# Optimization experiments

Hardware: AMD Instinct MI355X
Metric: run time of the kernel (lower is better)

The kernel has to match this reference:

```python
import jax, jax.numpy as jnp
import numpy as np
from jax import lax

B, N, C = 1, 4096, 256
NUM_HEADS, TOP_K = 8, 8
HID = 4 * C  # MSFN hidden_dim
EPS = 1e-5


def layer_norm(x, g, b):
    mu = jnp.mean(x, axis=-1, keepdims=True)
    var = jnp.mean((x - mu) ** 2, axis=-1, keepdims=True)
    return (x - mu) / jnp.sqrt(var + EPS) * g + b


def dwconv(x, w, b, pad):
    # x: [B,C,H,W]; w: [O,1,k,k] with feature_group_count=C (torch groups=dim)
    y = lax.conv_general_dilated(x, w, (1, 1), [(pad, pad), (pad, pad)],
                                 feature_group_count=C,
                                 dimension_numbers=("NCHW", "OIHW", "NCHW"))
    return y + b[None, :, None, None]


def setup_inputs() -> dict:
    key = jax.random.key(0)
    ks = jax.random.split(key, 12)
    std = 0.02
    inp = {
        "x": jax.random.normal(ks[0], (B, N, C), jnp.float32),
        "H": 64,
        "W": 64,
        "ln1_g": jnp.ones((C,), jnp.float32),
        "ln1_b": jnp.zeros((C,), jnp.float32),
        "q_w": jax.random.normal(ks[1], (C, C), jnp.float32) * std,
        "q_b": jnp.zeros((C,), jnp.float32),
        "kv_w": jax.random.normal(ks[2], (C, 2 * C), jnp.float32) * std,
        "kv_b": jnp.zeros((2 * C,), jnp.float32),
        "proj_w": jax.random.normal(ks[3], (C, C), jnp.float32) * std,
        "proj_b": jnp.zeros((C,), jnp.float32),
        "ln2_g": jnp.ones((C,), jnp.float32),
        "ln2_b": jnp.zeros((C,), jnp.float32),
        "conv3_w": jax.random.normal(ks[4], (HID, 1, 3, 3), jnp.float32) * np.sqrt(2.0 / (HID * 9 / C)),
        "conv3_b": jnp.zeros((HID,), jnp.float32),
        "conv5_w": jax.random.normal(ks[5], (HID, 1, 5, 5), jnp.float32) * np.sqrt(2.0 / (HID * 25 / C)),
        "conv5_b": jnp.zeros((HID,), jnp.float32),
        "conv1_w": jax.random.normal(ks[6], (C, 2 * HID, 1, 1), jnp.float32) * np.sqrt(2.0 / (C + 2 * HID)),
        "conv1_b": jnp.zeros((C,), jnp.float32),
    }
    return inp


def reference(x, H, W, ln1_g, ln1_b, q_w, q_b, kv_w, kv_b, proj_w, proj_b,
              ln2_g, ln2_b, conv3_w, conv3_b, conv5_w, conv5_b, conv1_w, conv1_b):
    Bh, Nn, Cc = x.shape
    D = Cc // NUM_HEADS
    scale = D ** -0.5

    # --- Dynamic sparse attention ---
    h = layer_norm(x, ln1_g, ln1_b)
    q = jax.nn.relu((h @ q_w + q_b).reshape(Bh, Nn, NUM_HEADS, D).transpose(0, 2, 1, 3))
    kv = (h @ kv_w + kv_b).reshape(Bh, Nn, 2, NUM_HEADS, D).transpose(2, 0, 3, 1, 4)
    k, v = kv[0], kv[1]  # [B,heads,N,D]
    attn = jnp.einsum("bhnd,bhmd->bhnm", q, k) * scale  # full dense map
    _, idx = lax.top_k(attn, TOP_K)  # [B,heads,N,k]
    bi = jnp.arange(Bh)[:, None, None, None]
    hi = jnp.arange(NUM_HEADS)[None, :, None, None]
    ni = jnp.arange(Nn)[None, None, :, None]
    mask = jnp.zeros_like(attn).at[bi, hi, ni, idx].set(1.0)
    # NOTE: matches torch exactly: non-topk entries become 0 (not -inf) pre-softmax
    sa = jax.nn.softmax(attn * mask, axis=-1)
    out = jnp.einsum("bhnm,bhmd->bhnd", sa, v).transpose(0, 2, 1, 3).reshape(Bh, Nn, Cc)
    x = x + (out @ proj_w + proj_b)

    # --- MSFN ---
    h2 = layer_norm(x, ln2_g, ln2_b)
    img = h2.transpose(0, 2, 1).reshape(Bh, Cc, H, W)
    x3 = jax.nn.relu(dwconv(img, conv3_w, conv3_b, 1))
    x5 = jax.nn.relu(dwconv(img, conv5_w, conv5_b, 2))
    cat = jnp.concatenate([x3, x5], axis=1)
    y = lax.conv_general_dilated(cat, conv1_w, (1, 1), [(0, 0), (0, 0)],
                                 dimension_numbers=("NCHW", "OIHW", "NCHW"))
    y = y + conv1_b[None, :, None, None]
    x = x + y.reshape(Bh, Cc, Nn).transpose(0, 2, 1)
    return x
```

## Files before the change

### kernel.cpp

```cpp
#include <hip/hip_runtime.h>
#include <math.h>

#define N_TOK 4096
#define C_DIM 256
#define HEADS 8
#define HDIM  32
#define SCALE 0.17677669529663687f

typedef float f32x4 __attribute__((ext_vector_type(4)));
typedef float f32x2 __attribute__((ext_vector_type(2)));
typedef int   i32x4 __attribute__((ext_vector_type(4)));
typedef __bf16 bf16x8 __attribute__((ext_vector_type(8)));
typedef __bf16 bf16x2 __attribute__((ext_vector_type(2)));

#if defined(__has_builtin)
#if __has_builtin(__builtin_amdgcn_mfma_f32_16x16x32_bf16)
#define HAVE_MFMA_BUILTIN 1
#endif
#if __has_builtin(__builtin_amdgcn_fdot2_f32_bf16)
#define HAVE_DOT2 1
#endif
#endif

__device__ __forceinline__ unsigned short f2bf(float x){
  unsigned u = __float_as_uint(x);
  u += 0x7FFFu + ((u >> 16) & 1u);
  return (unsigned short)(u >> 16);
}

__device__ __forceinline__ size_t pk_idx(int m, int k, int KT){
  return ((size_t)(m >> 4)*KT + (k >> 5))*512 + (((m & 15) + 16*((k >> 3) & 3))*8 + (k & 7));
}

__device__ __forceinline__ unsigned f2key(float s){
  unsigned b = __float_as_uint(s);
  return b ^ ((unsigned)((int)b >> 31) | 0x80000000u);
}
__device__ __forceinline__ unsigned umax_(unsigned a, unsigned b){ return a > b ? a : b; }
__device__ __forceinline__ unsigned umin_(unsigned a, unsigned b){ return a < b ? a : b; }

#define KCMP(A,i,j) { unsigned h_ = umax_(A[i],A[j]); unsigned l_ = umin_(A[i],A[j]); A[i]=h_; A[j]=l_; }

__device__ __forceinline__ void sort8(unsigned (&k)[8]){
  KCMP(k,0,1) KCMP(k,2,3) KCMP(k,4,5) KCMP(k,6,7)
  KCMP(k,0,2) KCMP(k,1,3) KCMP(k,4,6) KCMP(k,5,7)
  KCMP(k,1,2) KCMP(k,5,6)
  KCMP(k,0,4) KCMP(k,1,5) KCMP(k,2,6) KCMP(k,3,7)
  KCMP(k,2,4) KCMP(k,3,5)
  KCMP(k,1,2) KCMP(k,3,4) KCMP(k,5,6)
}

__device__ __forceinline__ void mergetop8(unsigned (&a)[8], const unsigned (&b)[8]){
  #pragma unroll
  for (int j=0;j<8;++j) a[j] = umax_(a[j], b[7-j]);
  KCMP(a,0,4) KCMP(a,1,5) KCMP(a,2,6) KCMP(a,3,7)
  KCMP(a,0,2) KCMP(a,1,3) KCMP(a,4,6) KCMP(a,5,7)
  KCMP(a,0,1) KCMP(a,2,3) KCMP(a,4,5) KCMP(a,6,7)
}

template<int MLO, int MHI>
__device__ __forceinline__ void merge_keys(unsigned (&k)[8]){
  #pragma unroll
  for (int m=MLO; m<=MHI; m<<=1){
    unsigned o[8];
    #pragma unroll
    for (int j=0;j<8;++j) o[j] = (unsigned)__shfl_xor((int)k[j], m);
    #pragma unroll
    for (int j=0;j<8;++j) k[j] = umax_(k[j], o[7-j]);
    KCMP(k,0,4) KCMP(k,1,5) KCMP(k,2,6) KCMP(k,3,7)
    KCMP(k,0,2) KCMP(k,1,3) KCMP(k,4,6) KCMP(k,5,7)
    KCMP(k,0,1) KCMP(k,2,3) KCMP(k,4,5) KCMP(k,6,7)
  }
}

__device__ __forceinline__ f32x4 mfma16(i32x4 a, i32x4 b, f32x4 c){
#ifdef HAVE_MFMA_BUILTIN
  return __builtin_amdgcn_mfma_f32_16x16x32_bf16(
      __builtin_bit_cast(bf16x8, a), __builtin_bit_cast(bf16x8, b), c, 0, 0, 0);
#else
  f32x4 d;
  asm volatile("v_mfma_f32_16x16x32_bf16 %0, %1, %2, %3\n\ts_nop 7\n\ts_nop 3"
               : "=&v"(d) : "v"(a), "v"(b), "v"(c));
  return d;
#endif
}

#ifdef HAVE_DOT2
struct QCtx { unsigned q[16]; };
__device__ __forceinline__ void qload(QCtx& qc, const unsigned short* qrow){
  #pragma unroll
  for (int i=0;i<4;++i){
    i32x4 qv = *(const i32x4*)(qrow + i*8);
    #pragma unroll
    for (int j=0;j<4;++j) qc.q[i*4+j] = (unsigned)qv[j];
  }
}
__device__ __forceinline__ float dot32(const i32x4& k0, const i32x4& k1,
                                       const i32x4& k2, const i32x4& k3, const QCtx& qc){
  float s = 0.f;
  #pragma unroll
  for (int q=0;q<4;++q){
    const i32x4& kv = (q==0)?k0 : (q==1)?k1 : (q==2)?k2 : k3;
    #pragma unroll
    for (int j=0;j<4;++j)
      s = __builtin_amdgcn_fdot2_f32_bf16(__builtin_bit_cast(bf16x2, (unsigned)kv[j]),
                                          __builtin_bit_cast(bf16x2, qc.q[q*4+j]), s, false);
  }
  return s;
}
#else
struct QCtx { f32x2 q[16]; };
__device__ __forceinline__ void qload(QCtx& qc, const unsigned short* qrow){
  #pragma unroll
  for (int i=0;i<4;++i){
    i32x4 qv = *(const i32x4*)(qrow + i*8);
    #pragma unroll
    for (int j=0;j<4;++j){
      unsigned u = (unsigned)qv[j];
      f32x2 p; p.x = __uint_as_float(u << 16); p.y = __uint_as_float(u & 0xFFFF0000u);
      qc.q[i*4+j] = p;
    }
  }
}
__device__ __forceinline__ float dot32(const i32x4& k0, const i32x4& k1,
                                       const i32x4& k2, const i32x4& k3, const QCtx& qc){
  f32x2 acc = {0.f, 0.f};
  #pragma unroll
  for (int q=0;q<4;++q){
    const i32x4& kv = (q==0)?k0 : (q==1)?k1 : (q==2)?k2 : k3;
    #pragma unroll
    for (int j=0;j<4;++j){
      unsigned u = (unsigned)kv[j];
      f32x2 p; p.x = __uint_as_float(u << 16); p.y = __uint_as_float(u & 0xFFFF0000u);
      acc += p * qc.q[q*4+j];
    }
  }
  return acc.x + acc.y;
}
#endif

template<int TO_PACK>
__global__ __launch_bounds__(256) void ln_kernel(const float* __restrict__ x,
    const float* __restrict__ g, const float* __restrict__ b,
    float* __restrict__ outF, unsigned short* __restrict__ outP)
{
  int row = blockIdx.x, c = threadIdx.x;
  float v = x[(size_t)row*C_DIM + c];
  float s1 = v, s2 = v*v;
  #pragma unroll
  for (int off=1; off<64; off<<=1){
    s1 += __shfl_xor(s1, off);
    s2 += __shfl_xor(s2, off);
  }
  __shared__ float r1[4], r2[4];
  int wv = c >> 6;
  if ((c & 63) == 0){ r1[wv] = s1; r2[wv] = s2; }
  __syncthreads();
  s1 = r1[0]+r1[1]+r1[2]+r1[3];
  s2 = r2[0]+r2[1]+r2[2]+r2[3];
  float mu  = s1 * (1.0f/C_DIM);
  float var = s2 * (1.0f/C_DIM) - mu*mu;
  float inv = 1.0f / sqrtf(var + 1e-5f);
  float o = (v - mu) * inv * g[c] + b[c];
  if (TO_PACK) outP[pk_idx(row, c, 8)] = f2bf(o);
  else         outF[(size_t)row*C_DIM + c] = o;
}

__global__ __launch_bounds__(256) void transpose_k(const float* __restrict__ src,
    float* __restrict__ dstF, int R, int Cc)
{
  __shared__ float t[64][65];
  int c0 = blockIdx.x*64, r0 = blockIdx.y*64;
  int x = threadIdx.x & 63, ys = threadIdx.x >> 6;
  #pragma unroll
  for (int i=0;i<16;++i){
    int r = ys + i*4;
    t[r][x] = src[(size_t)(r0+r)*Cc + c0 + x];
  }
  __syncthreads();
  #pragma unroll
  for (int i=0;i<16;++i){
    int rr = ys + i*4;
    dstF[(size_t)(c0+rr)*R + r0 + x] = t[x][rr];
  }
}

__global__ __launch_bounds__(256) void transpose_pack(const float* __restrict__ src,
    unsigned short* __restrict__ dstP, int Cc, int nbase, int KT)
{
  __shared__ float t[64][65];
  int c0 = blockIdx.x*64, r0 = blockIdx.y*64;
  int x = threadIdx.x & 63, ys = threadIdx.x >> 6;
  #pragma unroll
  for (int i=0;i<16;++i){
    int r = ys + i*4;
    t[r][x] = src[(size_t)(r0+r)*Cc + c0 + x];
  }
  __syncthreads();
  #pragma unroll
  for (int i=0;i<16;++i){
    int rr = ys + i*4;
    int n = nbase + c0 + rr;
    int k = r0 + x;
    dstP[pk_idx(n, k, KT)] = f2bf(t[x][rr]);
  }
}

__global__ __launch_bounds__(256) void pack_w1(const float* __restrict__ w1,
                                               unsigned short* __restrict__ w1p)
{
  int blk = blockIdx.x;
  int tid = threadIdx.x;
  int lane = tid >> 2;
  int j = (tid & 3) * 2;
  int n = (blk >> 6)*16 + (lane & 15);
  int k = (blk & 63)*32 + (lane >> 4)*8 + j;
  unsigned lo = f2bf(w1[(size_t)n*2048 + k]);
  unsigned hi = f2bf(w1[(size_t)n*2048 + k + 1]);
  *(unsigned*)(w1p + (size_t)blk*512 + lane*8 + j) = lo | (hi << 16);
}

#define LDT(p, i) (*(const i32x4*)((p) + (size_t)(i)*512))

template<int KTT, int KTC, int NPAIR>
__global__ __launch_bounds__(128, 2) void gemm_packed(
    const unsigned short* __restrict__ Ap, const unsigned short* __restrict__ Bp,
    const float* __restrict__ bias, const float* __restrict__ resid,
    float* __restrict__ outF, float* __restrict__ pbuf)
{
  int wave = threadIdx.x >> 6, lane = threadIdx.x & 63;
  int l16 = lane & 15, lg = lane >> 4;
  int mt = blockIdx.x*2 + wave;
  int nt0 = blockIdx.y * NPAIR;
  int z = blockIdx.z;
  const unsigned short* ap  = Ap + ((size_t)mt*KTT  + z*KTC)*512 + lane*8;
  const unsigned short* bp0 = Bp + ((size_t)nt0*KTT + z*KTC)*512 + lane*8;
  const unsigned short* bp1 = Bp + ((size_t)(nt0+1)*KTT + z*KTC)*512 + lane*8;
  f32x4 acc0 = {0.f,0.f,0.f,0.f}, acc1 = acc0;

  i32x4 A0 = LDT(ap,0), A1 = LDT(ap,1), A2 = LDT(ap,2), A3 = LDT(ap,3);
  i32x4 B0 = LDT(bp0,0), B1 = LDT(bp0,1), B2 = LDT(bp0,2), B3 = LDT(bp0,3);
  i32x4 C0, C1, C2, C3;
  if (NPAIR == 2){ C0 = LDT(bp1,0); C1 = LDT(bp1,1); C2 = LDT(bp1,2); C3 = LDT(bp1,3); }
  #pragma unroll
  for (int kt = 0; kt < KTC; ++kt){
    const int nk = (kt + 4 < KTC) ? (kt + 4) : (KTC - 1);
    switch (kt & 3){
      case 0: acc0 = mfma16(A0, B0, acc0); if (NPAIR==2) acc1 = mfma16(A0, C0, acc1);
              A0 = LDT(ap,nk); B0 = LDT(bp0,nk); if (NPAIR==2) C0 = LDT(bp1,nk); break;
      case 1: acc0 = mfma16(A1, B1, acc0); if (NPAIR==2) acc1 = mfma16(A1, C1, acc1);
              A1 = LDT(ap,nk); B1 = LDT(bp0,nk); if (NPAIR==2) C1 = LDT(bp1,nk); break;
      case 2: acc0 = mfma16(A2, B2, acc0); if (NPAIR==2) acc1 = mfma16(A2, C2, acc1);
              A2 = LDT(ap,nk); B2 = LDT(bp0,nk); if (NPAIR==2) C2 = LDT(bp1,nk); break;
      case 3: acc0 = mfma16(A3, B3, acc0); if (NPAIR==2) acc1 = mfma16(A3, C3, acc1);
              A3 = LDT(ap,nk); B3 = LDT(bp0,nk); if (NPAIR==2) C3 = LDT(bp1,nk); break;
    }
  }
  if (pbuf){
    float* pb = pbuf + (size_t)z * (N_TOK*C_DIM);
    #pragma unroll
    for (int f=0; f<NPAIR; ++f){
      f32x4 acc = f ? acc1 : acc0;
      int n = (nt0 + f)*16 + l16;
      #pragma unroll
      for (int r=0;r<4;++r)
        pb[(size_t)(mt*16 + lg*4 + r)*C_DIM + n] = acc[r];
    }
  } else {
    #pragma unroll
    for (int f=0; f<NPAIR; ++f){
      f32x4 acc = f ? acc1 : acc0;
      int n = (nt0 + f)*16 + l16;
      float bb = bias[n];
      #pragma unroll
      for (int r=0;r<4;++r){
        int m = mt*16 + lg*4 + r;
        float val = acc[r] + bb;
        if (resid) val += resid[(size_t)m*C_DIM + n];
        outF[(size_t)m*C_DIM + n] = val;
      }
    }
  }
}

__global__ __launch_bounds__(128, 2) void gemm_qkv_packed(
    const unsigned short* __restrict__ Ap, const unsigned short* __restrict__ Bp,
    const float* __restrict__ q_b, const float* __restrict__ kv_b,
    unsigned short* __restrict__ qbf, unsigned short* __restrict__ kbf,
    float* __restrict__ vbuf, unsigned short* __restrict__ kpackW)
{
  int wave = threadIdx.x >> 6, lane = threadIdx.x & 63;
  int l16 = lane & 15, lg = lane >> 4;
  int mt = blockIdx.x*2 + wave;
  int nt0 = blockIdx.y * 2;
  const unsigned short* ap  = Ap + ((size_t)mt*8)*512 + lane*8;
  const unsigned short* bp0 = Bp + ((size_t)nt0*8)*512 + lane*8;
  const unsigned short* bp1 = Bp + ((size_t)(nt0+1)*8)*512 + lane*8;
  f32x4 acc0 = {0.f,0.f,0.f,0.f}, acc1 = acc0;
  i32x4 A0 = LDT(ap,0), A1 = LDT(ap,1), A2 = LDT(ap,2), A3 = LDT(ap,3);
  i32x4 B0 = LDT(bp0,0), B1 = LDT(bp0,1), B2 = LDT(bp0,2), B3 = LDT(bp0,3);
  i32x4 C0 = LDT(bp1,0), C1 = LDT(bp1,1), C2 = LDT(bp1,2), C3 = LDT(bp1,3);
  #pragma unroll
  for (int kt = 0; kt < 8; ++kt){
    const int nk = (kt + 4 < 8) ? (kt + 4) : 7;
    switch (kt & 3){
      case 0: acc0 = mfma16(A0, B0, acc0); acc1 = mfma16(A0, C0, acc1);
              A0 = LDT(ap,nk); B0 = LDT(bp0,nk); C0 = LDT(bp1,nk); break;
      case 1: acc0 = mfma16(A1, B1, acc0); acc1 = mfma16(A1, C1, acc1);
              A1 = LDT(ap,nk); B1 = LDT(bp0,nk); C1 = LDT(bp1,nk); break;
      case 2: acc0 = mfma16(A2, B2, acc0); acc1 = mfma16(A2, C2, acc1);
              A2 = LDT(ap,nk); B2 = LDT(bp0,nk); C2 = LDT(bp1,nk); break;
      case 3: acc0 = mfma16(A3, B3, acc0); acc1 = mfma16(A3, C3, acc1);
              A3 = LDT(ap,nk); B3 = LDT(bp0,nk); C3 = LDT(bp1,nk); break;
    }
  }
  #pragma unroll
  for (int f=0; f<2; ++f){
    f32x4 acc = f ? acc1 : acc0;
    int n = (nt0 + f)*16 + l16;
    float bb = (n < 256) ? q_b[n] : kv_b[n-256];
    #pragma unroll
    for (int r=0;r<4;++r){
      int m = mt*16 + lg*4 + r;
      float val = acc[r] + bb;
      if (n < 256){
        qbf[(size_t)m*C_DIM + n] = f2bf(fmaxf(val, 0.f));
      } else if (n < 512){
        int ch = n - 256;
        unsigned short bv = f2bf(val);
        kbf[(size_t)m*C_DIM + ch] = bv;
        kpackW[((size_t)((ch >> 5)*256 + mt)*64 + (lg*4 + r) + 16*((ch >> 3) & 3))*8 + (ch & 7)] = bv;
      } else {
        vbuf[(size_t)m*C_DIM + (n-512)] = val;
      }
    }
  }
}

__global__ __launch_bounds__(256) void reduce_conv1(const float* __restrict__ pbuf,
    const float* __restrict__ bias, const float* __restrict__ resid,
    float* __restrict__ out)
{
  int i = (blockIdx.x*256 + threadIdx.x) * 4;
  f32x4 a = *(const f32x4*)(pbuf + i);
  f32x4 b = *(const f32x4*)(pbuf + (size_t)N_TOK*C_DIM + i);
  f32x4 r = *(const f32x4*)(resid + i);
  f32x4 bb = *(const f32x4*)(bias + (i & 255));
  *(f32x4*)(out + i) = a + b + r + bb;
}

__global__ __launch_bounds__(256) void colsum_part(const float* __restrict__ v, float* __restrict__ part){
  int b = blockIdx.x, c = threadIdx.x;
  float s = 0.f;
  for (int r=0;r<64;++r) s += v[(size_t)(b*64+r)*C_DIM + c];
  part[b*C_DIM + c] = s;
}
__global__ __launch_bounds__(256) void colsum_final(const float* __restrict__ part, float* __restrict__ sumv){
  int c = threadIdx.x;
  float s = 0.f;
  for (int b=0;b<64;++b) s += part[b*C_DIM + c];
  sumv[c] = s;
}

__global__ __launch_bounds__(256, 4) void attn_kernel(
    const unsigned short* __restrict__ qbf, const unsigned short* __restrict__ kbf,
    const unsigned short* __restrict__ kpack,
    const float* __restrict__ v, const float* __restrict__ sumv,
    unsigned short* __restrict__ outp)
{
  const int head = blockIdx.y;
  const int tid  = threadIdx.x;
  const int wave = tid >> 6, lane = tid & 63;
  const int l16 = lane & 15, lg = lane >> 4;
  const int row0 = blockIdx.x * 32;

  __shared__ unsigned ls[4][2][16][8];
  __shared__ int   gsel[32][8];
  __shared__ float lds_e[32][8];
  __shared__ int   lds_idx[32][8];
  __shared__ float lds_rd[32];

  i32x4 qf0 = *(const i32x4*)(qbf + (size_t)(row0      + l16)*C_DIM + head*HDIM + lg*8);
  i32x4 qf1 = *(const i32x4*)(qbf + (size_t)(row0 + 16 + l16)*C_DIM + head*HDIM + lg*8);
  const f32x4 zacc = {0.f,0.f,0.f,0.f};
  const int tbase = wave * 64;
  const unsigned short* kp = kpack + ((size_t)(head*256 + tbase)*64 + lane)*8;

  i32x4 kr0 = *(const i32x4*)(kp);
  i32x4 kr1 = *(const i32x4*)(kp + 512);
  i32x4 kr2 = *(const i32x4*)(kp + 1024);
  i32x4 kr3 = *(const i32x4*)(kp + 1536);
  i32x4 kr4 = *(const i32x4*)(kp + 2048);
  i32x4 kr5 = *(const i32x4*)(kp + 2560);
  i32x4 kr6 = *(const i32x4*)(kp + 3072);
  i32x4 kr7 = *(const i32x4*)(kp + 3584);

  unsigned t0[8], t1[8], g80[8], g81[8];
  #pragma unroll
  for (int j=0;j<8;++j){ t0[j]=0u; t1[j]=0u; }
  const int codebase = 511 - wave*128 - lg;
  #pragma unroll
  for (int g = 0; g < 32; ++g){
    float gm0 = -3e38f, gm1 = -3e38f;
    #pragma unroll
    for (int u = 0; u < 2; ++u){
      const int t = g*2 + u;
      #define USE_SLOT(S) { \
        f32x4 a0 = mfma16(S, qf0, zacc); \
        f32x4 a1 = mfma16(S, qf1, zacc); \
        S = *(const i32x4*)(kp + (size_t)(t+8)*512); \
        gm0 = fmaxf(gm0, fmaxf(fmaxf(a0[0],a0[1]), fmaxf(a0[2],a0[3]))); \
        gm1 = fmaxf(gm1, fmaxf(fmaxf(a1[0],a1[1]), fmaxf(a1[2],a1[3]))); }
      switch (t & 7){
        case 0: USE_SLOT(kr0); break;
        case 1: USE_SLOT(kr1); break;
        case 2: USE_SLOT(kr2); break;
        case 3: USE_SLOT(kr3); break;
        case 4: USE_SLOT(kr4); break;
        case 5: USE_SLOT(kr5); break;
        case 6: USE_SLOT(kr6); break;
        case 7: USE_SLOT(kr7); break;
      }
      #undef USE_SLOT
    }
    unsigned code = (unsigned)(codebase - g*4);
    g80[g & 7] = (f2key(gm0) & 0xFFFFFE00u) | code;
    g81[g & 7] = (f2key(gm1) & 0xFFFFFE00u) | code;
    if ((g & 7) == 7){
      sort8(g80); mergetop8(t0, g80);
      sort8(g81); mergetop8(t1, g81);
    }
  }
  merge_keys<16,32>(t0);
  merge_keys<16,32>(t1);

  if (lg == 0){
    #pragma unroll
    for (int j=0;j<8;++j){ ls[wave][0][l16][j]=t0[j]; ls[wave][1][l16][j]=t1[j]; }
  }
  __syncthreads();

  if (wave < 2){
    unsigned mk[8];
    #pragma unroll
    for (int j=0;j<8;++j) mk[j] = ls[lg][wave][l16][j];
    merge_keys<16,32>(mk);
    if (lg == 0){
      #pragma unroll
      for (int j=0;j<8;++j){
        int gid = 511 - (int)(mk[j] & 511u);
        gsel[wave*16 + l16][j] = (gid >> 2)*32 + (gid & 3)*4;
      }
    }
  }
  __syncthreads();

  const int prow = tid >> 3;
  const int sub  = tid & 7;
  QCtx qc;
  qload(qc, qbf + (size_t)(row0 + prow)*C_DIM + head*HDIM);
  const int base = gsel[prow][sub];
  const unsigned short* kh = kbf + head*HDIM;
  #define COLOF(c) (base + (((c) >> 2) << 4) + ((c) & 3))
  unsigned sv[8];
  #pragma unroll
  for (int j=0;j<8;++j) sv[j] = 0u;
  i32x4 A0,A1,A2,A3, B0,B1,B2,B3;
  { const unsigned short* p = kh + (size_t)COLOF(0)*C_DIM;
    A0 = *(const i32x4*)(p); A1 = *(const i32x4*)(p+8); A2 = *(const i32x4*)(p+16); A3 = *(const i32x4*)(p+24); }
  { const unsigned short* p = kh + (size_t)COLOF(1)*C_DIM;
    B0 = *(const i32x4*)(p); B1 = *(const i32x4*)(p+8); B2 = *(const i32x4*)(p+16); B3 = *(const i32x4*)(p+24); }
  #pragma unroll
  for (int c = 0; c < 8; ++c){
    float s;
    if ((c & 1) == 0){
      s = dot32(A0,A1,A2,A3, qc);
      if (c + 2 < 8){
        const unsigned short* p = kh + (size_t)COLOF(c+2)*C_DIM;
        A0 = *(const i32x4*)(p); A1 = *(const i32x4*)(p+8); A2 = *(const i32x4*)(p+16); A3 = *(const i32x4*)(p+24);
      }
    } else {
      s = dot32(B0,B1,B2,B3, qc);
      if (c + 2 < 8){
        const unsigned short* p = kh + (size_t)COLOF(c+2)*C_DIM;
        B0 = *(const i32x4*)(p); B1 = *(const i32x4*)(p+8); B2 = *(const i32x4*)(p+16); B3 = *(const i32x4*)(p+24);
      }
    }
    int col = COLOF(c);
    unsigned kk = (f2key(s) & 0xFFFFF000u) | (unsigned)(4095 - col);
    #pragma unroll
    for (int j=0;j<8;++j){ unsigned h = umax_(sv[j], kk); kk = umin_(sv[j], kk); sv[j] = h; }
  }
  #undef COLOF
  merge_keys<1,4>(sv);

  {
    int col = 4095 - (int)(sv[sub] & 4095u);
    const unsigned short* krow = kh + (size_t)col*C_DIM;
    i32x4 k0 = *(const i32x4*)(krow);
    i32x4 k1 = *(const i32x4*)(krow+8);
    i32x4 k2 = *(const i32x4*)(krow+16);
    i32x4 k3 = *(const i32x4*)(krow+24);
    float s = dot32(k0,k1,k2,k3, qc);
    lds_e[prow][sub] = expm1f(s*SCALE);
    lds_idx[prow][sub] = col;
  }
  __syncthreads();

  if (tid < 32){
    float den = 4096.0f;
    #pragma unroll
    for (int j=0;j<8;++j) den += lds_e[tid][j];
    lds_rd[tid] = 1.0f / den;
  }
  __syncthreads();

  #pragma unroll
  for (int it=0; it<4; ++it){
    int flat = it*256 + tid;
    int rl = flat >> 5, d = flat & 31;
    float num = sumv[head*HDIM + d];
    #pragma unroll
    for (int j=0;j<8;++j)
      num += lds_e[rl][j] * v[(size_t)lds_idx[rl][j]*C_DIM + head*HDIM + d];
    int row = row0 + rl;
    outp[pk_idx(row, head*HDIM + d, 8)] = f2bf(num * lds_rd[rl]);
  }
}

__global__ __launch_bounds__(256) void dwconv_tiled(const float* __restrict__ img,
    const float* __restrict__ w3, const float* __restrict__ b3,
    const float* __restrict__ w5, const float* __restrict__ b5,
    unsigned short* __restrict__ apack)
{
  __shared__ float tile[8][513];
  int bx = blockIdx.x;
  int ic0 = bx * 8;
  int py0 = blockIdx.y * 4;
  int tid = threadIdx.x;

  #pragma unroll
  for (int i = 0; i < 16; ++i){
    int idx = i*256 + tid;
    int ch  = idx >> 9;
    int rem = idx & 511;
    int ry  = rem >> 6, x = rem & 63;
    int y   = py0 - 2 + ry;
    float v = (y >= 0 && y < 64) ? img[(size_t)(ic0+ch)*4096 + y*64 + x] : 0.f;
    tile[ch][ry*64 + x] = v;
  }
  __syncthreads();

  int o_l  = tid & 31;
  int p_l  = tid >> 5;
  int ic_l = o_l >> 2;
  int o3   = ic0*4 + o_l;
  const float* pl = tile[ic_l];

  float W3[9], W5[25];
  #pragma unroll
  for (int i=0;i<9;++i)  W3[i] = w3[o3*9+i];
  #pragma unroll
  for (int i=0;i<25;++i) W5[i] = w5[o3*25+i];
  float bb3 = b3[o3], bb5 = b5[o3];

  int lane_lo = 16*((o_l >> 3) & 3);
  int elem    = o_l & 7;

  #pragma unroll 4
  for (int it = 0; it < 32; ++it){
    int pp = it*8 + p_l;
    int ly = (pp >> 6) + 2;
    int x  = pp & 63;
    float a3 = bb3, a5 = bb5;
    #pragma unroll
    for (int dy=-2; dy<=2; ++dy){
      #pragma unroll
      for (int dx=-2; dx<=2; ++dx){
        int xx = x + dx;
        float iv = (xx >= 0 && xx < 64) ? pl[(ly+dy)*64 + xx] : 0.f;
        a5 += W5[(dy+2)*5 + dx+2] * iv;
        if (dy>=-1 && dy<=1 && dx>=-1 && dx<=1)
          a3 += W3[(dy+1)*3 + dx+1] * iv;
      }
    }
    int p = (py0 + (pp>>6))*64 + x;
    size_t ad3 = ((size_t)(p >> 4)*64 + bx)*512 + ((p & 15) + lane_lo)*8 + elem;
    apack[ad3]          = f2bf(fmaxf(a3, 0.f));
    apack[ad3 + 32*512] = f2bf(fmaxf(a5, 0.f));
  }
}

extern "C" void kernel_launch(void* const* d_in, const int* in_sizes, int n_in,
                              void* d_out, int out_size, void* d_ws, size_t ws_size,
                              hipStream_t stream)
{
  (void)in_sizes; (void)n_in; (void)out_size; (void)ws_size;
  const float* x      = (const float*)d_in[0];
  const float* ln1_g  = (const float*)d_in[3];
  const float* ln1_b  = (const float*)d_in[4];
  const float* q_w    = (const float*)d_in[5];
  const float* q_b    = (const float*)d_in[6];
  const float* kv_w   = (const float*)d_in[7];
  const float* kv_b   = (const float*)d_in[8];
  const float* proj_w = (const float*)d_in[9];
  const float* proj_b = (const float*)d_in[10];
  const float* ln2_g  = (const float*)d_in[11];
  const float* ln2_b  = (const float*)d_in[12];
  const float* w3     = (const float*)d_in[13];
  const float* b3     = (const float*)d_in[14];
  const float* w5     = (const float*)d_in[15];
  const float* b5     = (const float*)d_in[16];
  const float* w1     = (const float*)d_in[17];
  const float* b1     = (const float*)d_in[18];
  float* out = (float*)d_out;
  char* ws = (char*)d_ws;

  unsigned short* wAllP = (unsigned short*)(ws + 0x0);
  unsigned short* pwP   = (unsigned short*)(ws + 0x60000);
  unsigned short* w1P   = (unsigned short*)(ws + 0x80000);
  unsigned short* kpack = (unsigned short*)(ws + 0x180000);
  unsigned short* qbf   = (unsigned short*)(ws + 0x380000);
  unsigned short* kbf   = (unsigned short*)(ws + 0x580000);
  float*          vbuf  = (float*)(ws + 0x780000);
  unsigned short* opack = (unsigned short*)(ws + 0xB80000);
  float*          x2    = (float*)(ws + 0xD80000);
  unsigned short* hpack = (unsigned short*)(ws + 0xD80000);
  float*          sumv  = (float*)(ws + 0x1180000);
  float*          part  = (float*)(ws + 0x1190000);
  float*          h2    = (float*)(ws + 0x180000);
  float*          h2T   = (float*)(ws + 0x580000);
  float*          pbuf  = (float*)(ws + 0x180000);
  unsigned short* apack = (unsigned short*)(ws + 0x1200000);

  dim3 b256(256), b128(128);

  pack_w1<<<dim3(1024), b256, 0, stream>>>(w1, w1P);
  transpose_pack<<<dim3(4,4), b256, 0, stream>>>(q_w,   wAllP, 256, 0,   8);
  transpose_pack<<<dim3(8,4), b256, 0, stream>>>(kv_w,  wAllP, 512, 256, 8);
  transpose_pack<<<dim3(4,4), b256, 0, stream>>>(proj_w, pwP,  256, 0,   8);

  ln_kernel<1><<<dim3(4096), b256, 0, stream>>>(x, ln1_g, ln1_b, nullptr, hpack);
  gemm_qkv_packed<<<dim3(128,24), b128, 0, stream>>>(hpack, wAllP, q_b, kv_b, qbf, kbf, vbuf, kpack);
  colsum_part <<<dim3(64), b256, 0, stream>>>(vbuf, part);
  colsum_final<<<dim3(1),  b256, 0, stream>>>(part, sumv);
  attn_kernel<<<dim3(128,8), b256, 0, stream>>>(qbf, kbf, kpack, vbuf, sumv, opack);
  gemm_packed<8,8,2><<<dim3(128,8,1), b128, 0, stream>>>(opack, pwP, proj_b, x, x2, nullptr);

  ln_kernel<0><<<dim3(4096), b256, 0, stream>>>(x2, ln2_g, ln2_b, h2, nullptr);
  transpose_k<<<dim3(4,64), b256, 0, stream>>>(h2, h2T, 4096, 256);
  dwconv_tiled<<<dim3(32,16), b256, 0, stream>>>(h2T, w3, b3, w5, b5, apack);
  gemm_packed<64,32,2><<<dim3(128,8,2), b128, 0, stream>>>(apack, w1P, nullptr, nullptr, nullptr, pbuf);
  reduce_conv1<<<dim3(1024), b256, 0, stream>>>(pbuf, b1, x2, out);
}
```

Measured before the change: 135.6 us.

## Fuse LN2 apply into transpose and software-pipeline MFMA results in top-k scan

The second layer norm is split into a lightweight per-token stats kernel (one wave per token, vectorized loads), and the normalization is applied inside the transpose kernel. This removes the full-size h2 intermediate write and read. The attention top-k scan loop is restructured so each MFMA result is consumed one iteration later, overlapping the max-reduction and sort work with the next MFMA's latency. The cost is extra per-token mu/rstd loads in the transpose and more live registers in the attention kernel.

```diff
diff --git a/kernel.cpp b/kernel.cpp
--- a/kernel.cpp
+++ b/kernel.cpp
@@ -139,10 +139,9 @@
 }
 #endif
 
-template<int TO_PACK>
-__global__ __launch_bounds__(256) void ln_kernel(const float* __restrict__ x,
+__global__ __launch_bounds__(256) void ln_kernel_pack(const float* __restrict__ x,
     const float* __restrict__ g, const float* __restrict__ b,
-    float* __restrict__ outF, unsigned short* __restrict__ outP)
+    unsigned short* __restrict__ outP)
 {
   int row = blockIdx.x, c = threadIdx.x;
   float v = x[(size_t)row*C_DIM + c];
@@ -162,26 +161,51 @@
   float var = s2 * (1.0f/C_DIM) - mu*mu;
   float inv = 1.0f / sqrtf(var + 1e-5f);
   float o = (v - mu) * inv * g[c] + b[c];
-  if (TO_PACK) outP[pk_idx(row, c, 8)] = f2bf(o);
-  else         outF[(size_t)row*C_DIM + c] = o;
-}
-
-__global__ __launch_bounds__(256) void transpose_k(const float* __restrict__ src,
-    float* __restrict__ dstF, int R, int Cc)
+  outP[pk_idx(row, c, 8)] = f2bf(o);
+}
+
+__global__ __launch_bounds__(256) void ln_stats(const float* __restrict__ x,
+    float* __restrict__ mu, float* __restrict__ rstd)
+{
+  int token = blockIdx.x*4 + (threadIdx.x >> 6);
+  int lane = threadIdx.x & 63;
+  f32x4 v = *(const f32x4*)(x + (size_t)token*C_DIM + lane*4);
+  float s1 = v[0]+v[1]+v[2]+v[3];
+  float s2 = v[0]*v[0]+v[1]*v[1]+v[2]*v[2]+v[3]*v[3];
+  #pragma unroll
+  for (int off=1; off<64; off<<=1){
+    s1 += __shfl_xor(s1, off);
+    s2 += __shfl_xor(s2, off);
+  }
+  if (lane == 0){
+    float m = s1 * (1.0f/C_DIM);
+    float var = s2 * (1.0f/C_DIM) - m*m;
+    mu[token] = m;
+    rstd[token] = 1.0f / sqrtf(var + 1e-5f);
+  }
+}
+
+__global__ __launch_bounds__(256) void transpose_norm(const float* __restrict__ src,
+    const float* __restrict__ mu, const float* __restrict__ rstd,
+    const float* __restrict__ g, const float* __restrict__ b,
+    float* __restrict__ dstF)
 {
   __shared__ float t[64][65];
   int c0 = blockIdx.x*64, r0 = blockIdx.y*64;
   int x = threadIdx.x & 63, ys = threadIdx.x >> 6;
+  float gg = g[c0 + x], bb = b[c0 + x];
   #pragma unroll
   for (int i=0;i<16;++i){
     int r = ys + i*4;
-    t[r][x] = src[(size_t)(r0+r)*Cc + c0 + x];
+    int tok = r0 + r;
+    float v = src[(size_t)tok*C_DIM + c0 + x];
+    t[r][x] = (v - mu[tok]) * rstd[tok] * gg + bb;
   }
   __syncthreads();
   #pragma unroll
   for (int i=0;i<16;++i){
     int rr = ys + i*4;
-    dstF[(size_t)(c0+rr)*R + r0 + x] = t[x][rr];
+    dstF[(size_t)(c0+rr)*N_TOK + r0 + x] = t[x][rr];
   }
 }
 
@@ -399,18 +423,15 @@
   #pragma unroll
   for (int j=0;j<8;++j){ t0[j]=0u; t1[j]=0u; }
   const int codebase = 511 - wave*128 - lg;
-  #pragma unroll
-  for (int g = 0; g < 32; ++g){
-    float gm0 = -3e38f, gm1 = -3e38f;
-    #pragma unroll
-    for (int u = 0; u < 2; ++u){
-      const int t = g*2 + u;
+  float gm0 = -3e38f, gm1 = -3e38f;
+  f32x4 pa0 = zacc, pa1 = zacc, ca0 = zacc, ca1 = zacc;
+  #pragma unroll
+  for (int t = 0; t <= 64; ++t){
+    if (t < 64){
       #define USE_SLOT(S) { \
-        f32x4 a0 = mfma16(S, qf0, zacc); \
-        f32x4 a1 = mfma16(S, qf1, zacc); \
-        S = *(const i32x4*)(kp + (size_t)(t+8)*512); \
-        gm0 = fmaxf(gm0, fmaxf(fmaxf(a0[0],a0[1]), fmaxf(a0[2],a0[3]))); \
-        gm1 = fmaxf(gm1, fmaxf(fmaxf(a1[0],a1[1]), fmaxf(a1[2],a1[3]))); }
+        ca0 = mfma16(S, qf0, zacc); \
+        ca1 = mfma16(S, qf1, zacc); \
+        S = *(const i32x4*)(kp + (size_t)(t+8)*512); }
       switch (t & 7){
         case 0: USE_SLOT(kr0); break;
         case 1: USE_SLOT(kr1); break;
@@ -423,13 +444,23 @@
       }
       #undef USE_SLOT
     }
-    unsigned code = (unsigned)(codebase - g*4);
-    g80[g & 7] = (f2key(gm0) & 0xFFFFFE00u) | code;
-    g81[g & 7] = (f2key(gm1) & 0xFFFFFE00u) | code;
-    if ((g & 7) == 7){
-      sort8(g80); mergetop8(t0, g80);
-      sort8(g81); mergetop8(t1, g81);
-    }
+    if (t >= 1){
+      const int tt = t - 1;
+      gm0 = fmaxf(gm0, fmaxf(fmaxf(pa0[0],pa0[1]), fmaxf(pa0[2],pa0[3])));
+      gm1 = fmaxf(gm1, fmaxf(fmaxf(pa1[0],pa1[1]), fmaxf(pa1[2],pa1[3])));
+      if (tt & 1){
+        const int g = tt >> 1;
+        unsigned code = (unsigned)(codebase - g*4);
+        g80[g & 7] = (f2key(gm0) & 0xFFFFFE00u) | code;
+        g81[g & 7] = (f2key(gm1) & 0xFFFFFE00u) | code;
+        gm0 = -3e38f; gm1 = -3e38f;
+        if ((g & 7) == 7){
+          sort8(g80); mergetop8(t0, g80);
+          sort8(g81); mergetop8(t1, g81);
+        }
+      }
+    }
+    pa0 = ca0; pa1 = ca1;
   }
   merge_keys<16,32>(t0);
   merge_keys<16,32>(t1);
@@ -628,7 +659,8 @@
   unsigned short* hpack = (unsigned short*)(ws + 0xD80000);
   float*          sumv  = (float*)(ws + 0x1180000);
   float*          part  = (float*)(ws + 0x1190000);
-  float*          h2    = (float*)(ws + 0x180000);
+  float*          mu    = (float*)(ws + 0x11A0000);
+  float*          rstd  = (float*)(ws + 0x11A4000);
   float*          h2T   = (float*)(ws + 0x580000);
   float*          pbuf  = (float*)(ws + 0x180000);
   unsigned short* apack = (unsigned short*)(ws + 0x1200000);
@@ -640,15 +672,15 @@
   transpose_pack<<<dim3(8,4), b256, 0, stream>>>(kv_w,  wAllP, 512, 256, 8);
   transpose_pack<<<dim3(4,4), b256, 0, stream>>>(proj_w, pwP,  256, 0,   8);
 
-  ln_kernel<1><<<dim3(4096), b256, 0, stream>>>(x, ln1_g, ln1_b, nullptr, hpack);
+  ln_kernel_pack<<<dim3(4096), b256, 0, stream>>>(x, ln1_g, ln1_b, hpack);
   gemm_qkv_packed<<<dim3(128,24), b128, 0, stream>>>(hpack, wAllP, q_b, kv_b, qbf, kbf, vbuf, kpack);
   colsum_part <<<dim3(64), b256, 0, stream>>>(vbuf, part);
   colsum_final<<<dim3(1),  b256, 0, stream>>>(part, sumv);
   attn_kernel<<<dim3(128,8), b256, 0, stream>>>(qbf, kbf, kpack, vbuf, sumv, opack);
   gemm_packed<8,8,2><<<dim3(128,8,1), b128, 0, stream>>>(opack, pwP, proj_b, x, x2, nullptr);
 
-  ln_kernel<0><<<dim3(4096), b256, 0, stream>>>(x2, ln2_g, ln2_b, h2, nullptr);
-  transpose_k<<<dim3(4,64), b256, 0, stream>>>(h2, h2T, 4096, 256);
+  ln_stats<<<dim3(1024), b256, 0, stream>>>(x2, mu, rstd);
+  transpose_norm<<<dim3(4,64), b256, 0, stream>>>(x2, mu, rstd, ln2_g, ln2_b, h2T);
   dwconv_tiled<<<dim3(32,16), b256, 0, stream>>>(h2T, w3, b3, w5, b5, apack);
   gemm_packed<64,32,2><<<dim3(128,8,2), b128, 0, stream>>>(apack, w1P, nullptr, nullptr, nullptr, pbuf);
   reduce_conv1<<<dim3(1024), b256, 0, stream>>>(pbuf, b1, x2, out);
```

Result: slower. 319.4 us (+135.5%).
